# Optimization experiments

Hardware: AMD Instinct MI355X
Metric: run time of the kernel (lower is better)

The kernel has to match this reference:

```python
import jax, jax.numpy as jnp
import numpy as np

B_MOL = 512      # molecules in batch
A_PER = 64       # atoms per molecule (uniform -> scopes are regular)
EU_PER = 2 * A_PER   # undirected bonds per molecule (ring + skip ring)
ED_PER = 2 * EU_PER  # directed bonds per molecule
N_ATOMS = B_MOL * A_PER
N_DIR = B_MOL * ED_PER
AF, BF = 98, 111
H, HEADS, DEPTH, MLP = 256, 8, 10, 512
DK = H // HEADS
ATOM_OUT, BOND_OUT = 128, 32


def _graph_indices():
    ar = np.arange(A_PER)
    su = np.concatenate([ar, ar])
    du = np.concatenate([(ar + 1) % A_PER, (ar + 2) % A_PER])
    src = np.concatenate([su, du])   # directed: fwd then rev copies
    dst = np.concatenate([du, su])
    rev = np.concatenate([np.arange(EU_PER) + EU_PER, np.arange(EU_PER)])
    offa = (np.arange(B_MOL) * A_PER)[:, None]
    offb = (np.arange(B_MOL) * ED_PER)[:, None]
    b2a = (src[None] + offa).reshape(-1).astype(np.int32)
    b2t = (dst[None] + offa).reshape(-1).astype(np.int32)
    b2rev = (rev[None] + offb).reshape(-1).astype(np.int32)
    pairs = np.stack([(su[None] + offa).reshape(-1), (du[None] + offa).reshape(-1)], 1).astype(np.int32)
    return jnp.asarray(b2a), jnp.asarray(b2t), jnp.asarray(b2rev), jnp.asarray(pairs)


def setup_inputs() -> dict:
    key = jax.random.key(0)
    ks = jax.random.split(key, 24)
    g = lambda k, s: jax.random.normal(k, s, jnp.float32) / np.sqrt(s[0])
    b2a, b2t, b2rev, bond_pairs = _graph_indices()
    return {
        'f_atoms': jax.random.normal(ks[0], (N_ATOMS, AF), jnp.float32),
        'f_bonds': jax.random.normal(ks[1], (N_DIR, BF), jnp.float32),
        'prev_hid': jnp.zeros((N_ATOMS, H), jnp.float32),
        'b2a': b2a, 'b2t': b2t, 'b2rev': b2rev, 'bond_pairs': bond_pairs,
        'W_i': g(ks[2], (BF, H)), 'W_h': g(ks[3], (H, H)),
        'W_o': g(ks[4], (AF + H, H)), 'b_o': jnp.zeros((H,), jnp.float32),
        'Wq': g(ks[5], (H, H)), 'Wk': g(ks[6], (H, H)),
        'Wv': g(ks[7], (H, H)), 'Wattn': g(ks[8], (H, H)),
        'W_vv': jnp.eye(H, dtype=jnp.float32), 'W_vc': g(ks[9], (H, H)),
        'A1': g(ks[10], (H, MLP)), 'a1': jnp.zeros((MLP,), jnp.float32),
        'A2': g(ks[11], (MLP, ATOM_OUT)), 'a2': jnp.zeros((ATOM_OUT,), jnp.float32),
        'B1': g(ks[12], (2 * H, MLP)), 'b1': jnp.zeros((MLP,), jnp.float32),
        'B2': g(ks[13], (MLP, BOND_OUT)), 'b2b': jnp.zeros((BOND_OUT,), jnp.float32),
        'G1': g(ks[14], (H, MLP)), 'g1': jnp.zeros((MLP,), jnp.float32),
        'G2': g(ks[15], (MLP, 1)), 'g2': jnp.zeros((1,), jnp.float32),
    }


def reference(f_atoms, f_bonds, prev_hid, b2a, b2t, b2rev, bond_pairs,
              W_i, W_h, W_o, b_o, Wq, Wk, Wv, Wattn, W_vv, W_vc,
              A1, a1, A2, a2, B1, b1, B2, b2b, G1, g1, G2, g2):
    # ---- DMPNN encoder (directed bond messages) ----
    h0 = jax.nn.relu(f_bonds @ W_i)                     # [E_dir, H]
    h = h0
    for _ in range(DEPTH - 1):
        a_sum = jax.ops.segment_sum(h, b2t, num_segments=N_ATOMS)  # incoming msg per atom
        m = a_sum[b2a] - h[b2rev]                       # exclude reverse bond
        h = jax.nn.relu(h0 + m @ W_h)
    a_in = jax.ops.segment_sum(h, b2t, num_segments=N_ATOMS)
    a_feats = jax.nn.relu(jnp.concatenate([f_atoms, a_in], 1) @ W_o + b_o)  # [N, H]

    # ---- Global_Attention over per-molecule scopes (uniform sizes -> reshape) ----
    x = a_feats.reshape(B_MOL, A_PER, H)
    q = (x @ Wq).reshape(B_MOL, A_PER, HEADS, DK)
    k = (x @ Wk).reshape(B_MOL, A_PER, HEADS, DK)
    v = (x @ Wv).reshape(B_MOL, A_PER, HEADS, DK)
    scores = jnp.einsum('bqhd,bkhd->bhqk', q, k) / np.sqrt(DK)
    attn = jax.nn.softmax(scores, axis=-1)
    ctx = jnp.einsum('bhqk,bkhd->bqhd', attn, v).reshape(B_MOL, A_PER, H)
    a_feats = (x + ctx @ Wattn).reshape(N_ATOMS, H)     # residual MHA

    # ---- recurrent atom state update ----
    atom_feats = jax.nn.relu(prev_hid @ W_vv.T + a_feats @ W_vc.T)  # [N, H]

    # ---- gather-based readout heads ----
    bond_feats = jnp.concatenate([atom_feats[bond_pairs[:, 0]],
                                  atom_feats[bond_pairs[:, 1]]], axis=1)  # [E_und, 2H]
    graph_vecs = atom_feats.reshape(B_MOL, A_PER, H).sum(axis=1)          # [B, H]

    atom_outs = jax.nn.relu(atom_feats @ A1 + a1) @ A2 + a2   # [N, ATOM_OUT]
    bond_outs = jax.nn.relu(bond_feats @ B1 + b1) @ B2 + b2b  # [E_und, BOND_OUT]
    graph_outs = jax.nn.relu(graph_vecs @ G1 + g1) @ G2 + g2  # [B, 1]

    # per-molecule edit scores: [bond scores | atom scores | graph score]
    edit_scores = jnp.concatenate([bond_outs.reshape(B_MOL, -1),
                                   atom_outs.reshape(B_MOL, -1),
                                   graph_outs], axis=1)
    return edit_scores
```

## Files before the change

### kernel.cpp

```cpp
#include <hip/hip_runtime.h>
#include <cstdint>
#include <cstddef>

#define B_MOL 512
#define A_PER 64
#define ED_PER 256
#define N_ATOMS (B_MOL * A_PER)
#define N_DIR (B_MOL * ED_PER)
#define N_UND (B_MOL * 128)
#define HID 256
#define OUT_STRIDE 12289
#define AP 40
#define CP 72

typedef __attribute__((ext_vector_type(8))) short bf16x8;
typedef __attribute__((ext_vector_type(8))) unsigned short u16x8;
typedef __attribute__((ext_vector_type(4))) float f32x4;

#define MFMA(a, b, c) __builtin_amdgcn_mfma_f32_16x16x32_bf16(a, b, c, 0, 0, 0)

__device__ __forceinline__ float b2f(unsigned short s) {
  return __builtin_bit_cast(float, (unsigned)s << 16);
}
__device__ __forceinline__ void split2(float v, unsigned short& h, unsigned short& l) {
  unsigned ub = __builtin_bit_cast(unsigned, v);
  h = (unsigned short)(ub >> 16);
  float fh = __builtin_bit_cast(float, ub & 0xffff0000u);
  float r = v - fh;
  l = (unsigned short)(__builtin_bit_cast(unsigned, r) >> 16);
}
__device__ __forceinline__ unsigned short f2bf_rne(float v) {
  unsigned u = __builtin_bit_cast(unsigned, v);
  u += 0x7FFFu + ((u >> 16) & 1u);
  return (unsigned short)(u >> 16);
}
__device__ __forceinline__ int e_src(int e) {
  return (e < 64) ? e : (e < 128) ? (e - 64)
       : (e < 192) ? ((e - 127) & 63) : ((e - 190) & 63);
}

__global__ __launch_bounds__(256) void convAll(
    const float* Wi, const float* Wh, const float* Wo,
    const float* Wq, const float* Wk, const float* Wv,
    const float* Wattn, const float* Wvc, const float* Wvv,
    const float* A1, const float* A2, const float* B1, const float* B2,
    const float* fbF, unsigned short* fbT,
    unsigned short* WiTh, unsigned short* WiTl,
    unsigned short* WhTh, unsigned short* WhTl,
    unsigned short* WoTh, unsigned short* WoTl,
    unsigned short* WqkvTh, unsigned short* WqkvTl,
    unsigned short* WaTh, unsigned short* WaTl,
    unsigned short* WcvTh, unsigned short* WcvTl,
    unsigned short* A1Th, unsigned short* A1Tl,
    unsigned short* A2Th, unsigned short* A2Tl,
    unsigned short* B1Th, unsigned short* B1Tl,
    unsigned short* B2Th, unsigned short* B2Tl) {
  int b = blockIdx.x;
  if (b >= 3232) {
    int e = (b - 3232) * 32 + (threadIdx.x >> 3);
    int ks = (threadIdx.x & 7) * 16;
    const float* s = fbF + (size_t)e * 111;
    u16x8 o0 = {0,0,0,0,0,0,0,0}, o1 = {0,0,0,0,0,0,0,0};
#pragma unroll
    for (int z = 0; z < 8; ++z) {
      int k = ks + z;
      if (k < 111) o0[z] = f2bf_rne(s[k]);
    }
#pragma unroll
    for (int z = 0; z < 8; ++z) {
      int k = ks + 8 + z;
      if (k < 111) o1[z] = f2bf_rne(s[k]);
    }
    *(u16x8*)&fbT[(size_t)e * 128 + ks] = o0;
    *(u16x8*)&fbT[(size_t)e * 128 + ks + 8] = o1;
    return;
  }
  const float *src = nullptr, *src2 = nullptr;
  unsigned short *dh = nullptr, *dl = nullptr;
  int K = 256, N = 256, Kp = 256, mode = 0, n = 0;
  if (b < 2048) {
    int seg = b >> 8; n = b & 255;
    switch (seg) {
      case 0: src = Wi; dh = WiTh; dl = WiTl; K = 111; Kp = 128; break;
      case 1: src = Wh; dh = WhTh; dl = WhTl; break;
      case 2: src = Wo; dh = WoTh; dl = WoTl; K = 354; Kp = 384; mode = 1; break;
      case 3: src = Wq; dh = WqkvTh; dl = WqkvTl; break;
      case 4: src = Wk; dh = WqkvTh + 65536; dl = WqkvTl + 65536; break;
      case 5: src = Wv; dh = WqkvTh + 131072; dl = WqkvTl + 131072; break;
      case 6: src = Wattn; dh = WaTh; dl = WaTl; break;
      default: src = Wvc; src2 = Wvv; dh = WcvTh; dl = WcvTl; K = 512; Kp = 512; mode = 2; break;
    }
  } else if (b < 2560) { n = b - 2048; src = A1; dh = A1Th; dl = A1Tl; K = 256; N = 512; Kp = 256; }
  else if (b < 2688)   { n = b - 2560; src = A2; dh = A2Th; dl = A2Tl; K = 512; N = 128; Kp = 512; }
  else if (b < 3200)   { n = b - 2688; src = B1; dh = B1Th; dl = B1Tl; K = 512; N = 512; Kp = 512; }
  else                 { n = b - 3200; src = B2; dh = B2Th; dl = B2Tl; K = 512; N = 32;  Kp = 512; }
  for (int k = threadIdx.x; k < Kp; k += 256) {
    float v = 0.f;
    if (mode == 0) { if (k < K) v = src[(size_t)k * N + n]; }
    else if (mode == 1) {
      if (k < 256) v = src[(size_t)(98 + k) * 256 + n];
      else if (k < 354) v = src[(size_t)(k - 256) * 256 + n];
    } else {
      v = (k < 256) ? src[(size_t)n * 256 + k] : src2[(size_t)n * 256 + (k - 256)];
    }
    unsigned short h_, l_;
    split2(v, h_, l_);
    dh[(size_t)n * Kp + k] = h_;
    dl[(size_t)n * Kp + k] = l_;
  }
}

template <int AMODE>
__launch_bounds__(256, 3)
__global__ void mgemm(const void* Aa_, const void* Ab_, const void* Ac_, const void* Ad_,
                      const unsigned short* __restrict__ BTh,
                      const unsigned short* __restrict__ BTl, int ldb,
                      const unsigned short* addH, const unsigned short* addL,
                      const float* __restrict__ bias,
                      const float* __restrict__ abias,
                      void* outA, void* outB,
                      int M, int N, int K, int lda, int ldco, int outcol,
                      int relu, int outmode) {
  __shared__ unsigned short AsH[128 * AP], AsL[128 * AP];
  __shared__ unsigned short BsH[128 * AP], BsL[128 * AP];
  const int tid = threadIdx.x;
  const int lane = tid & 63;
  const int l15 = lane & 15, l4 = lane >> 4;
  const int w = tid >> 6;
  const int wr = (w >> 1) * 64, wc = (w & 1) * 64;
  const int tileM = blockIdx.x * 128, tileN = blockIdx.y * 128;
  const int srow = tid >> 1;
  const int sks = (tid & 1) * 16;

  int rem = N - tileN - wc;
  int bnMax = rem >= 64 ? 4 : (rem > 0 ? (rem >> 4) : 0);

  f32x4 zf = {0.f, 0.f, 0.f, 0.f};
  f32x4 acc[4][4];
#pragma unroll
  for (int i = 0; i < 4; ++i)
#pragma unroll
    for (int j = 0; j < 4; ++j) acc[i][j] = zf;

  const int nkb = (K + 31) >> 5;
  for (int kb = 0; kb < nkb; ++kb) {
    __syncthreads();
    const int k0 = kb * 32 + sks;
    {
      const int row = tileM + srow;
      if (AMODE == 6) {
        const unsigned short* Ah = (const unsigned short*)Aa_;
        size_t bse = (size_t)row * lda + k0;
        *(u16x8*)&AsH[srow * AP + sks]     = *(const u16x8*)&Ah[bse];
        *(u16x8*)&AsH[srow * AP + sks + 8] = *(const u16x8*)&Ah[bse + 8];
      } else if (AMODE == 1 || (AMODE == 3 && k0 < 256)) {
        const unsigned short* Ah = (const unsigned short*)Aa_;
        const unsigned short* Al = (const unsigned short*)Ab_;
        size_t bse = (AMODE == 3) ? ((size_t)row * 256 + k0)
                                  : ((size_t)row * lda + k0);
        *(u16x8*)&AsH[srow * AP + sks]     = *(const u16x8*)&Ah[bse];
        *(u16x8*)&AsH[srow * AP + sks + 8] = *(const u16x8*)&Ah[bse + 8];
        *(u16x8*)&AsL[srow * AP + sks]     = *(const u16x8*)&Al[bse];
        *(u16x8*)&AsL[srow * AP + sks + 8] = *(const u16x8*)&Al[bse + 8];
      } else if (AMODE == 5) {
        int mol = row >> 7, u = row & 127;
        int a0 = (u < 64) ? u : (u - 64);
        int a1v = (u < 64) ? ((u + 1) & 63) : ((u - 62) & 63);
        size_t p1 = (size_t)(mol * 64 + a0) * 512 + k0;
        size_t p2 = (size_t)(mol * 64 + a1v) * 512 + k0;
        const unsigned short* P1h = (const unsigned short*)Aa_;
        const unsigned short* P1l = (const unsigned short*)Ab_;
        const unsigned short* P2h = (const unsigned short*)Ac_;
        const unsigned short* P2l = (const unsigned short*)Ad_;
        u16x8 x1h[2] = {*(const u16x8*)&P1h[p1], *(const u16x8*)&P1h[p1 + 8]};
        u16x8 x1l[2] = {*(const u16x8*)&P1l[p1], *(const u16x8*)&P1l[p1 + 8]};
        u16x8 x2h[2] = {*(const u16x8*)&P2h[p2], *(const u16x8*)&P2h[p2 + 8]};
        u16x8 x2l[2] = {*(const u16x8*)&P2l[p2], *(const u16x8*)&P2l[p2 + 8]};
#pragma unroll
        for (int c = 0; c < 2; ++c) {
          u16x8 hv, lv;
#pragma unroll
          for (int z = 0; z < 8; ++z) {
            float v = b2f(x1h[c][z]) + b2f(x1l[c][z])
                    + b2f(x2h[c][z]) + b2f(x2l[c][z]) + abias[k0 + c * 8 + z];
            v = fmaxf(v, 0.f);
            unsigned short h_, l_;
            split2(v, h_, l_);
            hv[z] = h_; lv[z] = l_;
          }
          *(u16x8*)&AsH[srow * AP + sks + c * 8] = hv;
          *(u16x8*)&AsL[srow * AP + sks + c * 8] = lv;
        }
      } else {
        u16x8 hv0 = {0,0,0,0,0,0,0,0}, lv0 = {0,0,0,0,0,0,0,0};
        u16x8 hv1 = {0,0,0,0,0,0,0,0}, lv1 = {0,0,0,0,0,0,0,0};
#pragma unroll
        for (int z = 0; z < 16; ++z) {
          int k = k0 + z;
          float v = 0.f;
          if (AMODE == 0) {
            if (k < K) v = ((const float*)Aa_)[(size_t)row * lda + k];
          } else if (AMODE == 2) {
            if (k < 256) v = ((const float*)Aa_)[(size_t)row * 256 + k];
            else if (k < 354) v = ((const float*)Ab_)[(size_t)row * 98 + (k - 256)];
          } else {
            v = ((const float*)Ac_)[(size_t)row * 256 + (k - 256)];
          }
          unsigned short h_, l_;
          split2(v, h_, l_);
          if (z < 8) { hv0[z] = h_; lv0[z] = l_; }
          else       { hv1[z - 8] = h_; lv1[z - 8] = l_; }
        }
        *(u16x8*)&AsH[srow * AP + sks]     = hv0;
        *(u16x8*)&AsH[srow * AP + sks + 8] = hv1;
        *(u16x8*)&AsL[srow * AP + sks]     = lv0;
        *(u16x8*)&AsL[srow * AP + sks + 8] = lv1;
      }
    }
    {
      const int n = tileN + srow;
      if (n < N) {
        size_t bb = (size_t)n * ldb + k0;
        *(u16x8*)&BsH[srow * AP + sks]     = *(const u16x8*)&BTh[bb];
        *(u16x8*)&BsH[srow * AP + sks + 8] = *(const u16x8*)&BTh[bb + 8];
        *(u16x8*)&BsL[srow * AP + sks]     = *(const u16x8*)&BTl[bb];
        *(u16x8*)&BsL[srow * AP + sks + 8] = *(const u16x8*)&BTl[bb + 8];
      } else {
        u16x8 z8 = {0,0,0,0,0,0,0,0};
        *(u16x8*)&BsH[srow * AP + sks]     = z8;
        *(u16x8*)&BsH[srow * AP + sks + 8] = z8;
        *(u16x8*)&BsL[srow * AP + sks]     = z8;
        *(u16x8*)&BsL[srow * AP + sks + 8] = z8;
      }
    }
    __syncthreads();
    bf16x8 ah[4], al[4];
#pragma unroll
    for (int am = 0; am < 4; ++am) {
      int ar = wr + am * 16 + l15;
      ah[am] = *(const bf16x8*)&AsH[ar * AP + l4 * 8];
      if (AMODE != 6) al[am] = *(const bf16x8*)&AsL[ar * AP + l4 * 8];
    }
#pragma unroll
    for (int bn = 0; bn < 4; ++bn) {
      if (bn < bnMax) {
        int br = wc + bn * 16 + l15;
        bf16x8 bh = *(const bf16x8*)&BsH[br * AP + l4 * 8];
        bf16x8 bl = *(const bf16x8*)&BsL[br * AP + l4 * 8];
#pragma unroll
        for (int am = 0; am < 4; ++am) {
          acc[am][bn] = MFMA(ah[am], bh, acc[am][bn]);
          acc[am][bn] = MFMA(ah[am], bl, acc[am][bn]);
          if (AMODE != 6) acc[am][bn] = MFMA(al[am], bh, acc[am][bn]);
        }
      }
    }
  }

#pragma unroll
  for (int am = 0; am < 4; ++am) {
#pragma unroll
    for (int bn = 0; bn < 4; ++bn) {
      if (bn >= bnMax) continue;
      int col = tileN + wc + bn * 16 + l15;
      float bs = bias ? bias[col] : 0.f;
#pragma unroll
      for (int r = 0; r < 4; ++r) {
        size_t row = (size_t)tileM + wr + am * 16 + l4 * 4 + r;
        float v = acc[am][bn][r] + bs;
        if (addH) v += b2f(addH[row * 256 + col]) + b2f(addL[row * 256 + col]);
        if (relu) v = fmaxf(v, 0.f);
        if (outmode == 0) {
          unsigned short h_, l_;
          split2(v, h_, l_);
          ((unsigned short*)outA)[row * (size_t)ldco + col] = h_;
          ((unsigned short*)outB)[row * (size_t)ldco + col] = l_;
        } else if (outmode == 1) {
          ((float*)outA)[row * (size_t)ldco + outcol + col] = v;
        } else if (outmode == 2) {
          int mol = (int)(row >> 6), t = (int)(row & 63);
          ((float*)outA)[(size_t)mol * OUT_STRIDE + 4096 + t * 128 + col] = v;
        } else {
          int mol = (int)(row >> 7), u = (int)(row & 127);
          ((float*)outA)[(size_t)mol * OUT_STRIDE + u * 32 + col] = v;
        }
      }
    }
  }
}

__launch_bounds__(1024)
__global__ void msg_f4(float* h,
                       const unsigned short* __restrict__ WhTh,
                       const unsigned short* __restrict__ WhTl,
                       const unsigned short* __restrict__ WiTh,
                       const unsigned short* __restrict__ WiTl,
                       const unsigned short* __restrict__ fbT) {
  extern __shared__ char smem_[];
  unsigned short* AsC = (unsigned short*)smem_;
  unsigned short* BsC = (unsigned short*)(smem_ + 36864);
  const int tid = threadIdx.x;
  const int lane = tid & 63, l15 = lane & 15, l4 = lane >> 4;
  const int w = tid >> 6;
  const int wm = (w >> 2) * 64;
  const int wn = (w & 3) * 64;
  const int mol = blockIdx.x;
  const int arow = tid >> 2;
  const int aks = (tid & 3) * 8;

  f32x4 acc[4][4];
#pragma unroll
  for (int i = 0; i < 4; ++i)
#pragma unroll
    for (int j = 0; j < 4; ++j) acc[i][j] = (f32x4){0.f, 0.f, 0.f, 0.f};

  const int sA = e_src(arow);
  const int rvA = (arow < 128) ? (arow + 128) : (arow - 128);
  const int i0 = (sA + 63) & 63;
  const int i1 = 64 + ((sA + 62) & 63);
  const int i2 = 128 + sA;
  const int i3 = 192 + sA;
  const size_t hbase = (size_t)mol * 256 * 256;

  const size_t fbb = (size_t)(mol * 256 + arow) * 128;
  for (int kb = 0; kb < 4; ++kb) {
    __syncthreads();
    {
      *(u16x8*)&AsC[arow * CP + aks] = *(const u16x8*)&fbT[fbb + kb * 32 + aks];
    }
    {
      size_t bb = (size_t)arow * 128 + kb * 32 + aks;
      *(u16x8*)&BsC[arow * CP + aks]      = *(const u16x8*)&WiTh[bb];
      *(u16x8*)&BsC[arow * CP + 32 + aks] = *(const u16x8*)&WiTl[bb];
    }
    __syncthreads();
    bf16x8 ah[4];
#pragma unroll
    for (int am = 0; am < 4; ++am) {
      int ar = wm + am * 16 + l15;
      ah[am] = *(const bf16x8*)&AsC[ar * CP + l4 * 8];
    }
#pragma unroll
    for (int bn = 0; bn < 4; ++bn) {
      int br = wn + bn * 16 + l15;
      bf16x8 bh = *(const bf16x8*)&BsC[br * CP + l4 * 8];
      bf16x8 bl = *(const bf16x8*)&BsC[br * CP + 32 + l4 * 8];
#pragma unroll
      for (int am = 0; am < 4; ++am) {
        acc[am][bn] = MFMA(ah[am], bh, acc[am][bn]);
        acc[am][bn] = MFMA(ah[am], bl, acc[am][bn]);
      }
    }
  }
#pragma unroll
  for (int i = 0; i < 4; ++i)
#pragma unroll
    for (int j = 0; j < 4; ++j)
#pragma unroll
      for (int r = 0; r < 4; ++r) acc[i][j][r] = fmaxf(acc[i][j][r], 0.f);

  for (int kb = 0; kb < 8; ++kb) {
    __syncthreads();
    {
      const int c0 = kb * 32 + aks;
      f32x4 m0, m1;
      {
        const float* p = &h[hbase + (size_t)i0 * 256 + c0];
        m0 = *(const f32x4*)p;
        m1 = *(const f32x4*)(p + 4);
      }
      {
        const float* p = &h[hbase + (size_t)i1 * 256 + c0];
        m0 += *(const f32x4*)p;
        m1 += *(const f32x4*)(p + 4);
      }
      {
        const float* p = &h[hbase + (size_t)i2 * 256 + c0];
        m0 += *(const f32x4*)p;
        m1 += *(const f32x4*)(p + 4);
      }
      {
        const float* p = &h[hbase + (size_t)i3 * 256 + c0];
        m0 += *(const f32x4*)p;
        m1 += *(const f32x4*)(p + 4);
      }
      {
        const float* p = &h[hbase + (size_t)rvA * 256 + c0];
        m0 -= *(const f32x4*)p;
        m1 -= *(const f32x4*)(p + 4);
      }
      u16x8 hv, lv;
#pragma unroll
      for (int z = 0; z < 4; ++z) {
        unsigned short h_, l_;
        split2(m0[z], h_, l_); hv[z] = h_; lv[z] = l_;
        split2(m1[z], h_, l_); hv[4 + z] = h_; lv[4 + z] = l_;
      }
      *(u16x8*)&AsC[arow * CP + aks]      = hv;
      *(u16x8*)&AsC[arow * CP + 32 + aks] = lv;
    }
    {
      size_t bb = (size_t)arow * 256 + kb * 32 + aks;
      *(u16x8*)&BsC[arow * CP + aks]      = *(const u16x8*)&WhTh[bb];
      *(u16x8*)&BsC[arow * CP + 32 + aks] = *(const u16x8*)&WhTl[bb];
    }
    __syncthreads();
    bf16x8 ah[4], al[4];
#pragma unroll
    for (int am = 0; am < 4; ++am) {
      int ar = wm + am * 16 + l15;
      ah[am] = *(const bf16x8*)&AsC[ar * CP + l4 * 8];
      al[am] = *(const bf16x8*)&AsC[ar * CP + 32 + l4 * 8];
    }
#pragma unroll
    for (int bn = 0; bn < 4; ++bn) {
      int br = wn + bn * 16 + l15;
      bf16x8 bh = *(const bf16x8*)&BsC[br * CP + l4 * 8];
      bf16x8 bl = *(const bf16x8*)&BsC[br * CP + 32 + l4 * 8];
#pragma unroll
      for (int am = 0; am < 4; ++am) {
        acc[am][bn] = MFMA(ah[am], bh, acc[am][bn]);
        acc[am][bn] = MFMA(ah[am], bl, acc[am][bn]);
        acc[am][bn] = MFMA(al[am], bh, acc[am][bn]);
      }
    }
  }

#pragma unroll
  for (int am = 0; am < 4; ++am) {
#pragma unroll
    for (int r = 0; r < 4; ++r) {
      int row = wm + am * 16 + l4 * 4 + r;
      size_t rowb = hbase + (size_t)row * 256;
#pragma unroll
      for (int bn = 0; bn < 4; ++bn) {
        int col = wn + bn * 16 + l15;
        h[rowb + col] = fmaxf(acc[am][bn][r], 0.f);
      }
    }
  }
}

__global__ __launch_bounds__(256) void asum_f(const float* __restrict__ h,
                                              float* __restrict__ out) {
  int g = blockIdx.x * 256 + threadIdx.x;
  int atom = g >> 5, cc = (g & 31) << 3;
  int mol = atom >> 6, t = atom & 63;
  const float* hb = h + (size_t)mol * ED_PER * HID;
  int e0 = (t + 63) & 63;
  int e1 = 64 + ((t + 62) & 63);
  int e2 = 128 + t;
  int e3 = 192 + t;
  f32x4 s0 = {0.f, 0.f, 0.f, 0.f}, s1 = {0.f, 0.f, 0.f, 0.f};
#define ACC_E(ee) { \
    const float* p = hb + (size_t)(ee) * HID + cc; \
    s0 += *(const f32x4*)p; \
    s1 += *(const f32x4*)(p + 4); }
  ACC_E(e0); ACC_E(e1); ACC_E(e2); ACC_E(e3);
#undef ACC_E
  *(f32x4*)&out[(size_t)atom * HID + cc] = s0;
  *(f32x4*)&out[(size_t)atom * HID + cc + 4] = s1;
}

__global__ __launch_bounds__(64) void attn_k(const float* __restrict__ qkv,
                                             unsigned short* __restrict__ ctxH,
                                             unsigned short* __restrict__ ctxL) {
  __shared__ float kls[64 * 32];
  __shared__ float vls[64 * 32];
  int mol = blockIdx.x >> 3, head = blockIdx.x & 7;
  int lane = threadIdx.x;
  size_t rb = ((size_t)(mol * 64 + lane)) * 768 + head * 32;
#pragma unroll
  for (int c = 0; c < 8; ++c) {
    *(float4*)(kls + lane * 32 + c * 4) = *(const float4*)(qkv + rb + 256 + c * 4);
    *(float4*)(vls + lane * 32 + c * 4) = *(const float4*)(qkv + rb + 512 + c * 4);
  }
  float q[32];
#pragma unroll
  for (int d = 0; d < 32; ++d) q[d] = qkv[rb + d];
  __syncthreads();
  float mx = -1e30f, l = 0.f;
  float acc[32];
#pragma unroll
  for (int d = 0; d < 32; ++d) acc[d] = 0.f;
  for (int j = 0; j < 64; ++j) {
    float s = 0.f;
#pragma unroll
    for (int d = 0; d < 32; ++d) s += q[d] * kls[j * 32 + d];
    s *= 0.17677669529663687f;
    float nm = fmaxf(mx, s);
    float co = __expf(mx - nm);
    float p = __expf(s - nm);
    l = l * co + p;
#pragma unroll
    for (int d = 0; d < 32; ++d) acc[d] = acc[d] * co + p * vls[j * 32 + d];
    mx = nm;
  }
  float inv = 1.f / l;
  size_t ob = ((size_t)(mol * 64 + lane)) * 256 + head * 32;
#pragma unroll
  for (int d = 0; d < 32; ++d) {
    unsigned short h_, l_;
    split2(acc[d] * inv, h_, l_);
    ctxH[ob + d] = h_;
    ctxL[ob + d] = l_;
  }
}

__global__ __launch_bounds__(256) void gv_k(const unsigned short* __restrict__ afH,
                                            const unsigned short* __restrict__ afL,
                                            float* __restrict__ gv) {
  int mol = blockIdx.x, c = threadIdx.x;
  float s = 0.f;
  for (int a = 0; a < 64; ++a) {
    size_t i = ((size_t)mol * 64 + a) * 256 + c;
    s += b2f(afH[i]) + b2f(afL[i]);
  }
  gv[mol * 256 + c] = s;
}

__global__ __launch_bounds__(512) void gh_k(const float* __restrict__ gv, const float* __restrict__ G1,
                                            const float* __restrict__ g1, const float* __restrict__ G2,
                                            const float* __restrict__ g2, float* __restrict__ out) {
  __shared__ float xs[256];
  __shared__ float red[512];
  int mol = blockIdx.x, j = threadIdx.x;
  if (j < 256) xs[j] = gv[mol * 256 + j];
  __syncthreads();
  float s = 0.f;
  for (int k = 0; k < 256; ++k) s += xs[k] * G1[k * 512 + j];
  s = fmaxf(s + g1[j], 0.f);
  red[j] = s * G2[j];
  __syncthreads();
  for (int st = 256; st > 0; st >>= 1) {
    if (j < st) red[j] += red[j + st];
    __syncthreads();
  }
  if (j == 0) out[(size_t)mol * OUT_STRIDE + 12288] = red[0] + g2[0];
}

extern "C" void kernel_launch(void* const* d_in, const int* in_sizes, int n_in,
                              void* d_out, int out_size, void* d_ws, size_t ws_size,
                              hipStream_t stream) {
  (void)in_sizes; (void)n_in; (void)out_size; (void)ws_size;
  const float* f_atoms  = (const float*)d_in[0];
  const float* f_bonds  = (const float*)d_in[1];
  const float* prev_hid = (const float*)d_in[2];
  const float* W_i   = (const float*)d_in[7];
  const float* W_h   = (const float*)d_in[8];
  const float* W_o   = (const float*)d_in[9];
  const float* b_o   = (const float*)d_in[10];
  const float* Wq    = (const float*)d_in[11];
  const float* Wk    = (const float*)d_in[12];
  const float* Wv    = (const float*)d_in[13];
  const float* Wattn = (const float*)d_in[14];
  const float* W_vv  = (const float*)d_in[15];
  const float* W_vc  = (const float*)d_in[16];
  const float* A1    = (const float*)d_in[17];
  const float* a1    = (const float*)d_in[18];
  const float* A2    = (const float*)d_in[19];
  const float* a2    = (const float*)d_in[20];
  const float* B1    = (const float*)d_in[21];
  const float* b1    = (const float*)d_in[22];
  const float* B2    = (const float*)d_in[23];
  const float* b2b   = (const float*)d_in[24];
  const float* G1    = (const float*)d_in[25];
  const float* g1    = (const float*)d_in[26];
  const float* G2    = (const float*)d_in[27];
  const float* g2    = (const float*)d_in[28];
  float* out = (float*)d_out;

  char* base = (char*)d_ws;
  float* h = (float*)(base);
  unsigned short* fbT = (unsigned short*)(base + 134217728);
  float* asumF = (float*)(base + 134217728);
  char* W0 = base + 167772160;
  unsigned short* WiTh   = (unsigned short*)(W0);
  unsigned short* WiTl   = (unsigned short*)(W0 + 65536);
  unsigned short* WhTh   = (unsigned short*)(W0 + 131072);
  unsigned short* WhTl   = (unsigned short*)(W0 + 262144);
  unsigned short* WoTh   = (unsigned short*)(W0 + 393216);
  unsigned short* WoTl   = (unsigned short*)(W0 + 589824);
  unsigned short* WqkvTh = (unsigned short*)(W0 + 786432);
  unsigned short* WqkvTl = (unsigned short*)(W0 + 1179648);
  unsigned short* WaTh   = (unsigned short*)(W0 + 1572864);
  unsigned short* WaTl   = (unsigned short*)(W0 + 1703936);
  unsigned short* WcvTh  = (unsigned short*)(W0 + 1835008);
  unsigned short* WcvTl  = (unsigned short*)(W0 + 2097152);
  unsigned short* A1Th   = (unsigned short*)(W0 + 2359296);
  unsigned short* A1Tl   = (unsigned short*)(W0 + 2621440);
  unsigned short* A2Th   = (unsigned short*)(W0 + 2883584);
  unsigned short* A2Tl   = (unsigned short*)(W0 + 3014656);
  unsigned short* B1Th   = (unsigned short*)(W0 + 3145728);
  unsigned short* B1Tl   = (unsigned short*)(W0 + 3670016);
  unsigned short* B2Th   = (unsigned short*)(W0 + 4194304);
  unsigned short* B2Tl   = (unsigned short*)(W0 + 4227072);
  float* gvec            = (float*)(W0 + 4259840);
  unsigned short* xAh  = (unsigned short*)(base);
  unsigned short* xAl  = (unsigned short*)(base + 16777216);
  float* qkv           = (float*)(base + 33554432);
  unsigned short* ctxh = (unsigned short*)(base + 134217728);
  unsigned short* ctxl = (unsigned short*)(base + 150994944);
  unsigned short* afh  = (unsigned short*)(base + 33554432);
  unsigned short* afl  = (unsigned short*)(base + 50331648);
  unsigned short* atfh = (unsigned short*)(base + 67108864);
  unsigned short* atfl = (unsigned short*)(base + 83886080);
  unsigned short* t1h  = (unsigned short*)(base);
  unsigned short* t1l  = (unsigned short*)(base + 33554432);
  unsigned short* P1h  = (unsigned short*)(base);
  unsigned short* P1l  = (unsigned short*)(base + 33554432);
  unsigned short* P2h  = (unsigned short*)(base + 100663296);
  unsigned short* P2l  = (unsigned short*)(base + 134217728);

  convAll<<<7328, 256, 0, stream>>>(
      W_i, W_h, W_o, Wq, Wk, Wv, Wattn, W_vc, W_vv, A1, A2, B1, B2,
      f_bonds, fbT,
      WiTh, WiTl, WhTh, WhTl, WoTh, WoTl, WqkvTh, WqkvTl, WaTh, WaTl,
      WcvTh, WcvTl, A1Th, A1Tl, A2Th, A2Tl, B1Th, B1Tl, B2Th, B2Tl);

  mgemm<6><<<dim3(1024, 2), 256, 0, stream>>>(
      fbT, nullptr, nullptr, nullptr, WiTh, WiTl, 128,
      nullptr, nullptr, nullptr, nullptr,
      h, nullptr, N_DIR, 256, 128, 128, 256, 0, 1, 1);

  for (int d = 0; d < 9; ++d) {
    msg_f4<<<512, 1024, 73728, stream>>>(h, WhTh, WhTl, WiTh, WiTl, fbT);
  }

  asum_f<<<4096, 256, 0, stream>>>(h, asumF);
  mgemm<2><<<dim3(256, 2), 256, 0, stream>>>(
      asumF, f_atoms, nullptr, nullptr, WoTh, WoTl, 384,
      nullptr, nullptr, b_o, nullptr,
      xAh, xAl, N_ATOMS, 256, 354, 0, 256, 0, 1, 0);
  mgemm<1><<<dim3(256, 6), 256, 0, stream>>>(
      xAh, xAl, nullptr, nullptr, WqkvTh, WqkvTl, 256,
      nullptr, nullptr, nullptr, nullptr,
      qkv, nullptr, N_ATOMS, 768, 256, 256, 768, 0, 0, 1);
  attn_k<<<4096, 64, 0, stream>>>(qkv, ctxh, ctxl);
  mgemm<1><<<dim3(256, 2), 256, 0, stream>>>(
      ctxh, ctxl, nullptr, nullptr, WaTh, WaTl, 256,
      xAh, xAl, nullptr, nullptr,
      afh, afl, N_ATOMS, 256, 256, 256, 256, 0, 0, 0);
  mgemm<3><<<dim3(256, 2), 256, 0, stream>>>(
      afh, afl, prev_hid, nullptr, WcvTh, WcvTl, 512,
      nullptr, nullptr, nullptr, nullptr,
      atfh, atfl, N_ATOMS, 256, 512, 256, 256, 0, 1, 0);
  mgemm<1><<<dim3(256, 4), 256, 0, stream>>>(
      atfh, atfl, nullptr, nullptr, A1Th, A1Tl, 256,
      nullptr, nullptr, a1, nullptr,
      t1h, t1l, N_ATOMS, 512, 256, 256, 512, 0, 1, 0);
  mgemm<1><<<dim3(256, 1), 256, 0, stream>>>(
      t1h, t1l, nullptr, nullptr, A2Th, A2Tl, 512,
      nullptr, nullptr, a2, nullptr,
      out, nullptr, N_ATOMS, 128, 512, 512, 0, 0, 0, 2);
  mgemm<1><<<dim3(256, 4), 256, 0, stream>>>(
      atfh, atfl, nullptr, nullptr, B1Th, B1Tl, 512,
      nullptr, nullptr, nullptr, nullptr,
      P1h, P1l, N_ATOMS, 512, 256, 256, 512, 0, 0, 0);
  mgemm<1><<<dim3(256, 4), 256, 0, stream>>>(
      atfh, atfl, nullptr, nullptr, B1Th + 256, B1Tl + 256, 512,
      nullptr, nullptr, nullptr, nullptr,
      P2h, P2l, N_ATOMS, 512, 256, 256, 512, 0, 0, 0);
  mgemm<5><<<dim3(512, 1), 256, 0, stream>>>(
      P1h, P1l, P2h, P2l, B2Th, B2Tl, 512,
      nullptr, nullptr, b2b, b1,
      out, nullptr, N_UND, 32, 512, 0, 0, 0, 0, 3);
  gv_k<<<512, 256, 0, stream>>>(atfh, atfl, gvec);
  gh_k<<<512, 512, 0, stream>>>(gvec, G1, g1, G2, g2, out);
}
```

Measured before the change: 1.794 ms.

## Fold attention output projection into state-update GEMM and merge B1 GEMMs

Precomputes Wattn·W_vc^T so the context projection and recurrent update become one K=768 GEMM over [ctx | x | prev_hid]. This removes a separate GEMM launch and the round trip of the intermediate a_feats. The two B1 half-GEMMs are merged into one N=1024 GEMM whose interleaved output the bond-pair gather kernel reads directly. The trade-off is a per-block 256-length dot-product loop in the weight conversion kernel, and a change in rounding order from the pre-multiplied weights.

```diff
diff --git a/kernel.cpp b/kernel.cpp
--- a/kernel.cpp
+++ b/kernel.cpp
@@ -50,14 +50,14 @@
     unsigned short* WoTh, unsigned short* WoTl,
     unsigned short* WqkvTh, unsigned short* WqkvTl,
     unsigned short* WaTh, unsigned short* WaTl,
-    unsigned short* WcvTh, unsigned short* WcvTl,
+    unsigned short* Wcv2Th, unsigned short* Wcv2Tl,
     unsigned short* A1Th, unsigned short* A1Tl,
     unsigned short* A2Th, unsigned short* A2Tl,
-    unsigned short* B1Th, unsigned short* B1Tl,
+    unsigned short* B1bTh, unsigned short* B1bTl,
     unsigned short* B2Th, unsigned short* B2Tl) {
   int b = blockIdx.x;
-  if (b >= 3232) {
-    int e = (b - 3232) * 32 + (threadIdx.x >> 3);
+  if (b >= 3744) {
+    int e = (b - 3744) * 32 + (threadIdx.x >> 3);
     int ks = (threadIdx.x & 7) * 16;
     const float* s = fbF + (size_t)e * 111;
     u16x8 o0 = {0,0,0,0,0,0,0,0}, o1 = {0,0,0,0,0,0,0,0};
@@ -75,34 +75,71 @@
     *(u16x8*)&fbT[(size_t)e * 128 + ks + 8] = o1;
     return;
   }
-  const float *src = nullptr, *src2 = nullptr;
+  if (b >= 1792 && b < 2048) {
+    int n = b & 255;
+    for (int k = threadIdx.x; k < 768; k += 256) {
+      float v;
+      if (k < 256) {
+        v = 0.f;
+        for (int j = 0; j < 256; ++j)
+          v += Wattn[(size_t)k * 256 + j] * Wvc[(size_t)n * 256 + j];
+      } else if (k < 512) {
+        v = Wvc[(size_t)n * 256 + (k - 256)];
+      } else {
+        v = Wvv[(size_t)n * 256 + (k - 512)];
+      }
+      unsigned short h_, l_;
+      split2(v, h_, l_);
+      Wcv2Th[(size_t)n * 768 + k] = h_;
+      Wcv2Tl[(size_t)n * 768 + k] = l_;
+    }
+    return;
+  }
+  if (b >= 2688 && b < 3712) {
+    int n = b - 2688;
+    int k = threadIdx.x;
+    float v = (n < 512) ? B1[(size_t)k * 512 + n]
+                        : B1[(size_t)(k + 256) * 512 + (n - 512)];
+    unsigned short h_, l_;
+    split2(v, h_, l_);
+    B1bTh[(size_t)n * 256 + k] = h_;
+    B1bTl[(size_t)n * 256 + k] = l_;
+    return;
+  }
+  const float* src = nullptr;
   unsigned short *dh = nullptr, *dl = nullptr;
-  int K = 256, N = 256, Kp = 256, mode = 0, n = 0;
-  if (b < 2048) {
+  int K = 256, N = 256, Kp = 256, n = 0;
+  if (b < 1792) {
     int seg = b >> 8; n = b & 255;
     switch (seg) {
       case 0: src = Wi; dh = WiTh; dl = WiTl; K = 111; Kp = 128; break;
       case 1: src = Wh; dh = WhTh; dl = WhTl; break;
-      case 2: src = Wo; dh = WoTh; dl = WoTl; K = 354; Kp = 384; mode = 1; break;
+      case 2: src = Wo; dh = WoTh; dl = WoTl; K = 354; Kp = 384; break;
       case 3: src = Wq; dh = WqkvTh; dl = WqkvTl; break;
       case 4: src = Wk; dh = WqkvTh + 65536; dl = WqkvTl + 65536; break;
       case 5: src = Wv; dh = WqkvTh + 131072; dl = WqkvTl + 131072; break;
-      case 6: src = Wattn; dh = WaTh; dl = WaTl; break;
-      default: src = Wvc; src2 = Wvv; dh = WcvTh; dl = WcvTl; K = 512; Kp = 512; mode = 2; break;
-    }
-  } else if (b < 2560) { n = b - 2048; src = A1; dh = A1Th; dl = A1Tl; K = 256; N = 512; Kp = 256; }
-  else if (b < 2688)   { n = b - 2560; src = A2; dh = A2Th; dl = A2Tl; K = 512; N = 128; Kp = 512; }
-  else if (b < 3200)   { n = b - 2688; src = B1; dh = B1Th; dl = B1Tl; K = 512; N = 512; Kp = 512; }
-  else                 { n = b - 3200; src = B2; dh = B2Th; dl = B2Tl; K = 512; N = 32;  Kp = 512; }
+      default: src = Wattn; dh = WaTh; dl = WaTl; break;
+    }
+    for (int k = threadIdx.x; k < Kp; k += 256) {
+      float v = 0.f;
+      if (b >> 8 == 2) {
+        if (k < 256) v = src[(size_t)(98 + k) * 256 + n];
+        else if (k < 354) v = src[(size_t)(k - 256) * 256 + n];
+      } else {
+        if (k < K) v = src[(size_t)k * N + n];
+      }
+      unsigned short h_, l_;
+      split2(v, h_, l_);
+      dh[(size_t)n * Kp + k] = h_;
+      dl[(size_t)n * Kp + k] = l_;
+    }
+    return;
+  }
+  if (b < 2560)      { n = b - 2048; src = A1; dh = A1Th; dl = A1Tl; K = 256; N = 512; Kp = 256; }
+  else if (b < 2688) { n = b - 2560; src = A2; dh = A2Th; dl = A2Tl; K = 512; N = 128; Kp = 512; }
+  else               { n = b - 3712; src = B2; dh = B2Th; dl = B2Tl; K = 512; N = 32;  Kp = 512; }
   for (int k = threadIdx.x; k < Kp; k += 256) {
-    float v = 0.f;
-    if (mode == 0) { if (k < K) v = src[(size_t)k * N + n]; }
-    else if (mode == 1) {
-      if (k < 256) v = src[(size_t)(98 + k) * 256 + n];
-      else if (k < 354) v = src[(size_t)(k - 256) * 256 + n];
-    } else {
-      v = (k < 256) ? src[(size_t)n * 256 + k] : src2[(size_t)n * 256 + (k - 256)];
-    }
+    float v = (k < K) ? src[(size_t)k * N + n] : 0.f;
     unsigned short h_, l_;
     split2(v, h_, l_);
     dh[(size_t)n * Kp + k] = h_;
@@ -113,6 +150,7 @@
 template <int AMODE>
 __launch_bounds__(256, 3)
 __global__ void mgemm(const void* Aa_, const void* Ab_, const void* Ac_, const void* Ad_,
+                      const float* __restrict__ Af32,
                       const unsigned short* __restrict__ BTh,
                       const unsigned short* __restrict__ BTl, int ldb,
                       const unsigned short* addH, const unsigned short* addL,
@@ -153,11 +191,18 @@
         size_t bse = (size_t)row * lda + k0;
         *(u16x8*)&AsH[srow * AP + sks]     = *(const u16x8*)&Ah[bse];
         *(u16x8*)&AsH[srow * AP + sks + 8] = *(const u16x8*)&Ah[bse + 8];
-      } else if (AMODE == 1 || (AMODE == 3 && k0 < 256)) {
-        const unsigned short* Ah = (const unsigned short*)Aa_;
-        const unsigned short* Al = (const unsigned short*)Ab_;
-        size_t bse = (AMODE == 3) ? ((size_t)row * 256 + k0)
-                                  : ((size_t)row * lda + k0);
+      } else if (AMODE == 1 || (AMODE == 7 && k0 < 512)) {
+        const unsigned short* Ah; const unsigned short* Al;
+        size_t bse;
+        if (AMODE == 7) {
+          Ah = (k0 < 256) ? (const unsigned short*)Aa_ : (const unsigned short*)Ac_;
+          Al = (k0 < 256) ? (const unsigned short*)Ab_ : (const unsigned short*)Ad_;
+          bse = (size_t)row * 256 + (k0 & 255);
+        } else {
+          Ah = (const unsigned short*)Aa_;
+          Al = (const unsigned short*)Ab_;
+          bse = (size_t)row * lda + k0;
+        }
         *(u16x8*)&AsH[srow * AP + sks]     = *(const u16x8*)&Ah[bse];
         *(u16x8*)&AsH[srow * AP + sks + 8] = *(const u16x8*)&Ah[bse + 8];
         *(u16x8*)&AsL[srow * AP + sks]     = *(const u16x8*)&Al[bse];
@@ -166,16 +211,14 @@
         int mol = row >> 7, u = row & 127;
         int a0 = (u < 64) ? u : (u - 64);
         int a1v = (u < 64) ? ((u + 1) & 63) : ((u - 62) & 63);
-        size_t p1 = (size_t)(mol * 64 + a0) * 512 + k0;
-        size_t p2 = (size_t)(mol * 64 + a1v) * 512 + k0;
-        const unsigned short* P1h = (const unsigned short*)Aa_;
-        const unsigned short* P1l = (const unsigned short*)Ab_;
-        const unsigned short* P2h = (const unsigned short*)Ac_;
-        const unsigned short* P2l = (const unsigned short*)Ad_;
-        u16x8 x1h[2] = {*(const u16x8*)&P1h[p1], *(const u16x8*)&P1h[p1 + 8]};
-        u16x8 x1l[2] = {*(const u16x8*)&P1l[p1], *(const u16x8*)&P1l[p1 + 8]};
-        u16x8 x2h[2] = {*(const u16x8*)&P2h[p2], *(const u16x8*)&P2h[p2 + 8]};
-        u16x8 x2l[2] = {*(const u16x8*)&P2l[p2], *(const u16x8*)&P2l[p2 + 8]};
+        size_t p1 = (size_t)(mol * 64 + a0) * 1024 + k0;
+        size_t p2 = (size_t)(mol * 64 + a1v) * 1024 + 512 + k0;
+        const unsigned short* Ph = (const unsigned short*)Aa_;
+        const unsigned short* Pl = (const unsigned short*)Ab_;
+        u16x8 x1h[2] = {*(const u16x8*)&Ph[p1], *(const u16x8*)&Ph[p1 + 8]};
+        u16x8 x1l[2] = {*(const u16x8*)&Pl[p1], *(const u16x8*)&Pl[p1 + 8]};
+        u16x8 x2h[2] = {*(const u16x8*)&Ph[p2], *(const u16x8*)&Ph[p2 + 8]};
+        u16x8 x2l[2] = {*(const u16x8*)&Pl[p2], *(const u16x8*)&Pl[p2 + 8]};
 #pragma unroll
         for (int c = 0; c < 2; ++c) {
           u16x8 hv, lv;
@@ -204,7 +247,7 @@
             if (k < 256) v = ((const float*)Aa_)[(size_t)row * 256 + k];
             else if (k < 354) v = ((const float*)Ab_)[(size_t)row * 98 + (k - 256)];
           } else {
-            v = ((const float*)Ac_)[(size_t)row * 256 + (k - 256)];
+            v = Af32[(size_t)row * 256 + (k - 512)];
           }
           unsigned short h_, l_;
           split2(v, h_, l_);
@@ -585,41 +628,37 @@
   unsigned short* WqkvTl = (unsigned short*)(W0 + 1179648);
   unsigned short* WaTh   = (unsigned short*)(W0 + 1572864);
   unsigned short* WaTl   = (unsigned short*)(W0 + 1703936);
-  unsigned short* WcvTh  = (unsigned short*)(W0 + 1835008);
-  unsigned short* WcvTl  = (unsigned short*)(W0 + 2097152);
-  unsigned short* A1Th   = (unsigned short*)(W0 + 2359296);
-  unsigned short* A1Tl   = (unsigned short*)(W0 + 2621440);
-  unsigned short* A2Th   = (unsigned short*)(W0 + 2883584);
-  unsigned short* A2Tl   = (unsigned short*)(W0 + 3014656);
-  unsigned short* B1Th   = (unsigned short*)(W0 + 3145728);
-  unsigned short* B1Tl   = (unsigned short*)(W0 + 3670016);
-  unsigned short* B2Th   = (unsigned short*)(W0 + 4194304);
-  unsigned short* B2Tl   = (unsigned short*)(W0 + 4227072);
-  float* gvec            = (float*)(W0 + 4259840);
+  unsigned short* Wcv2Th = (unsigned short*)(W0 + 1835008);
+  unsigned short* Wcv2Tl = (unsigned short*)(W0 + 2228224);
+  unsigned short* A1Th   = (unsigned short*)(W0 + 2621440);
+  unsigned short* A1Tl   = (unsigned short*)(W0 + 2883584);
+  unsigned short* A2Th   = (unsigned short*)(W0 + 3145728);
+  unsigned short* A2Tl   = (unsigned short*)(W0 + 3276800);
+  unsigned short* B1bTh  = (unsigned short*)(W0 + 3407872);
+  unsigned short* B1bTl  = (unsigned short*)(W0 + 3932160);
+  unsigned short* B2Th   = (unsigned short*)(W0 + 4456448);
+  unsigned short* B2Tl   = (unsigned short*)(W0 + 4489216);
+  float* gvec            = (float*)(W0 + 4521984);
   unsigned short* xAh  = (unsigned short*)(base);
   unsigned short* xAl  = (unsigned short*)(base + 16777216);
   float* qkv           = (float*)(base + 33554432);
   unsigned short* ctxh = (unsigned short*)(base + 134217728);
   unsigned short* ctxl = (unsigned short*)(base + 150994944);
-  unsigned short* afh  = (unsigned short*)(base + 33554432);
-  unsigned short* afl  = (unsigned short*)(base + 50331648);
   unsigned short* atfh = (unsigned short*)(base + 67108864);
   unsigned short* atfl = (unsigned short*)(base + 83886080);
   unsigned short* t1h  = (unsigned short*)(base);
   unsigned short* t1l  = (unsigned short*)(base + 33554432);
-  unsigned short* P1h  = (unsigned short*)(base);
-  unsigned short* P1l  = (unsigned short*)(base + 33554432);
-  unsigned short* P2h  = (unsigned short*)(base + 100663296);
-  unsigned short* P2l  = (unsigned short*)(base + 134217728);
-
-  convAll<<<7328, 256, 0, stream>>>(
+  unsigned short* Ph   = (unsigned short*)(base);
+  unsigned short* Pl   = (unsigned short*)(base + 100663296);
+
+  convAll<<<7840, 256, 0, stream>>>(
       W_i, W_h, W_o, Wq, Wk, Wv, Wattn, W_vc, W_vv, A1, A2, B1, B2,
       f_bonds, fbT,
       WiTh, WiTl, WhTh, WhTl, WoTh, WoTl, WqkvTh, WqkvTl, WaTh, WaTl,
-      WcvTh, WcvTl, A1Th, A1Tl, A2Th, A2Tl, B1Th, B1Tl, B2Th, B2Tl);
+      Wcv2Th, Wcv2Tl, A1Th, A1Tl, A2Th, A2Tl, B1bTh, B1bTl, B2Th, B2Tl);
 
   mgemm<6><<<dim3(1024, 2), 256, 0, stream>>>(
-      fbT, nullptr, nullptr, nullptr, WiTh, WiTl, 128,
+      fbT, nullptr, nullptr, nullptr, nullptr, WiTh, WiTl, 128,
       nullptr, nullptr, nullptr, nullptr,
       h, nullptr, N_DIR, 256, 128, 128, 256, 0, 1, 1);
 
@@ -629,40 +668,32 @@
 
   asum_f<<<4096, 256, 0, stream>>>(h, asumF);
   mgemm<2><<<dim3(256, 2), 256, 0, stream>>>(
-      asumF, f_atoms, nullptr, nullptr, WoTh, WoTl, 384,
+      asumF, f_atoms, nullptr, nullptr, nullptr, WoTh, WoTl, 384,
       nullptr, nullptr, b_o, nullptr,
       xAh, xAl, N_ATOMS, 256, 354, 0, 256, 0, 1, 0);
   mgemm<1><<<dim3(256, 6), 256, 0, stream>>>(
-      xAh, xAl, nullptr, nullptr, WqkvTh, WqkvTl, 256,
+      xAh, xAl, nullptr, nullptr, nullptr, WqkvTh, WqkvTl, 256,
       nullptr, nullptr, nullptr, nullptr,
       qkv, nullptr, N_ATOMS, 768, 256, 256, 768, 0, 0, 1);
   attn_k<<<4096, 64, 0, stream>>>(qkv, ctxh, ctxl);
-  mgemm<1><<<dim3(256, 2), 256, 0, stream>>>(
-      ctxh, ctxl, nullptr, nullptr, WaTh, WaTl, 256,
-      xAh, xAl, nullptr, nullptr,
-      afh, afl, N_ATOMS, 256, 256, 256, 256, 0, 0, 0);
-  mgemm<3><<<dim3(256, 2), 256, 0, stream>>>(
-      afh, afl, prev_hid, nullptr, WcvTh, WcvTl, 512,
+  mgemm<7><<<dim3(256, 2), 256, 0, stream>>>(
+      ctxh, ctxl, xAh, xAl, prev_hid, Wcv2Th, Wcv2Tl, 768,
       nullptr, nullptr, nullptr, nullptr,
-      atfh, atfl, N_ATOMS, 256, 512, 256, 256, 0, 1, 0);
+      atfh, atfl, N_ATOMS, 256, 768, 256, 256, 0, 1, 0);
   mgemm<1><<<dim3(256, 4), 256, 0, stream>>>(
-      atfh, atfl, nullptr, nullptr, A1Th, A1Tl, 256,
+      atfh, atfl, nullptr, nullptr, nullptr, A1Th, A1Tl, 256,
       nullptr, nullptr, a1, nullptr,
       t1h, t1l, N_ATOMS, 512, 256, 256, 512, 0, 1, 0);
   mgemm<1><<<dim3(256, 1), 256, 0, stream>>>(
-      t1h, t1l, nullptr, nullptr, A2Th, A2Tl, 512,
+      t1h, t1l, nullptr, nullptr, nullptr, A2Th, A2Tl, 512,
       nullptr, nullptr, a2, nullptr,
       out, nullptr, N_ATOMS, 128, 512, 512, 0, 0, 0, 2);
-  mgemm<1><<<dim3(256, 4), 256, 0, stream>>>(
-      atfh, atfl, nullptr, nullptr, B1Th, B1Tl, 512,
+  mgemm<1><<<dim3(256, 8), 256, 0, stream>>>(
+      atfh, atfl, nullptr, nullptr, nullptr, B1bTh, B1bTl, 256,
       nullptr, nullptr, nullptr, nullptr,
-      P1h, P1l, N_ATOMS, 512, 256, 256, 512, 0, 0, 0);
-  mgemm<1><<<dim3(256, 4), 256, 0, stream>>>(
-      atfh, atfl, nullptr, nullptr, B1Th + 256, B1Tl + 256, 512,
-      nullptr, nullptr, nullptr, nullptr,
-      P2h, P2l, N_ATOMS, 512, 256, 256, 512, 0, 0, 0);
+      Ph, Pl, N_ATOMS, 1024, 256, 256, 1024, 0, 0, 0);
   mgemm<5><<<dim3(512, 1), 256, 0, stream>>>(
-      P1h, P1l, P2h, P2l, B2Th, B2Tl, 512,
+      Ph, Pl, nullptr, nullptr, nullptr, B2Th, B2Tl, 512,
       nullptr, nullptr, b2b, b1,
       out, nullptr, N_UND, 32, 512, 0, 0, 0, 0, 3);
   gv_k<<<512, 256, 0, stream>>>(atfh, atfl, gvec);
```

Result: faster. 1.732 ms (-3.4%).
